# Performance work log

Hardware: AMD Instinct MI355X
Metric: run time of the kernel (lower is better)

## Reference

```python
import jax, jax.numpy as jnp
import numpy as np
from functools import partial

VOCAB = 32000
N_LAYER = 2
D_MODEL = 1024
D_INNER = 2048   # expand * d_model
D_STATE = 16
D_CONV = 4
DT_RANK = 64     # ceil(d_model/16)
SEQ_LEN = 2048   # == D_INNER (required by the repo's conv quirk)
BATCH = 1
EPS = 1e-6


def rmsnorm(x, scale):
    return x * jax.lax.rsqrt(jnp.mean(x * x, axis=-1, keepdims=True) + EPS) * scale


def setup_inputs() -> dict:
    key = jax.random.key(0)
    ks = jax.random.split(key, 16)
    s = 0.02
    L = N_LAYER
    inp = {
        "input_ids": jax.random.randint(ks[0], (BATCH, SEQ_LEN), 0, VOCAB, dtype=jnp.int32),
        "embed": jax.random.normal(ks[1], (VOCAB, D_MODEL), jnp.float32) * s,
        "norm_scale": jnp.ones((L, D_MODEL), jnp.float32),
        "in_proj_w": jax.random.normal(ks[2], (L, D_MODEL, 2 * D_INNER), jnp.float32) * s,
        "in_proj_b": jnp.zeros((L, 2 * D_INNER), jnp.float32),
        "conv_w": jax.random.normal(ks[3], (L, D_CONV, 1, SEQ_LEN), jnp.float32) * s,
        "conv_b": jnp.zeros((L, SEQ_LEN), jnp.float32),
        "x_proj_w": jax.random.normal(ks[4], (L, D_MODEL, DT_RANK + 2 * D_STATE), jnp.float32) * s,
        "dt_proj_w": jax.random.normal(ks[5], (L, DT_RANK, D_INNER), jnp.float32) * s,
        "dt_proj_b": jnp.zeros((L, D_INNER), jnp.float32),
        "out_proj_w": jax.random.normal(ks[6], (L, D_INNER, D_MODEL), jnp.float32) * s,
        "out_proj_b": jnp.zeros((L, D_MODEL), jnp.float32),
        "A_log": jnp.tile(jnp.log(jnp.arange(1, D_STATE + 1, dtype=jnp.float32)), (L, D_INNER, 1)),
        "D_param": jnp.ones((L, D_INNER), jnp.float32),
        "norm_f_scale": jnp.ones((D_MODEL,), jnp.float32),
        "lm_head_w": jax.random.normal(ks[7], (D_MODEL, VOCAB), jnp.float32) * s,
    }
    return inp


def selective_scan(u, delta, A, B, C, D):
    # u, delta: (b,l,d)   A: (d,n)   B,C: (b,l,n)   D: (d,)
    deltaA = jnp.exp(jnp.einsum('bld,dn->bldn', delta, A))            # (b,l,d,n)
    deltaB_u = delta[..., None] * B[:, :, None, :] * u[..., None]      # (b,l,d,n)

    def step(x, inps):
        dA, dBu, c = inps            # (b,d,n),(b,d,n),(b,n)
        x = dA * x + dBu
        y = jnp.einsum('bdn,bn->bd', x, c)
        return x, y

    x0 = jnp.zeros((u.shape[0], u.shape[2], A.shape[1]), u.dtype)
    _, ys = jax.lax.scan(step, x0, (jnp.moveaxis(deltaA, 1, 0),
                                    jnp.moveaxis(deltaB_u, 1, 0),
                                    jnp.moveaxis(C, 1, 0)))
    return jnp.moveaxis(ys, 0, 1) + u * D                              # (b,l,d)


def depthwise_conv(x, w, b):
    # Faithful to repo: Conv(features=SEQ_LEN, groups=D_INNER) on (b, d_inner, l).
    # With SEQ_LEN == D_INNER this is a depthwise conv over the d_inner axis.
    # x: (b, d_inner, l) as (N, W, C);  w: (d_conv, 1, SEQ_LEN)
    y = jax.lax.conv_general_dilated(x, w, window_strides=(1,), padding='SAME',
                                     dimension_numbers=('NWC', 'WIO', 'NWC'),
                                     feature_group_count=SEQ_LEN)
    return y + b


def mamba_block(h, norm_scale, in_w, in_b, conv_w, conv_b, x_proj_w,
                dt_w, dt_b, out_w, out_b, A_log, Dp):
    u = rmsnorm(h, norm_scale)
    A = -jnp.exp(A_log)
    x_and_res = u @ in_w + in_b
    x, res = jnp.split(x_and_res, 2, axis=-1)
    xt = jnp.transpose(x, (0, 2, 1))                 # (b, d_inner, l)
    xt = depthwise_conv(xt, conv_w, conv_b)[:, :, :u.shape[1]]
    x = jax.nn.silu(jnp.transpose(xt, (0, 2, 1)))     # (b, l, d_inner)
    x_dbl = u @ x_proj_w
    delta, B, C = jnp.split(x_dbl, [DT_RANK, DT_RANK + D_STATE], axis=-1)
    delta = jax.nn.softplus(delta @ dt_w + dt_b)
    y = selective_scan(x, delta, A, B, C, Dp)
    y = y * jax.nn.silu(res)
    return y @ out_w + out_b + h


def reference(input_ids, embed, norm_scale, in_proj_w, in_proj_b, conv_w, conv_b,
              x_proj_w, dt_proj_w, dt_proj_b, out_proj_w, out_proj_b, A_log,
              D_param, norm_f_scale, lm_head_w):
    h = embed[input_ids]                              # (b,l,d_model)
    for i in range(N_LAYER):
        h = mamba_block(h, norm_scale[i], in_proj_w[i], in_proj_b[i], conv_w[i],
                        conv_b[i], x_proj_w[i], dt_proj_w[i], dt_proj_b[i],
                        out_proj_w[i], out_proj_b[i], A_log[i], D_param[i])
    h = rmsnorm(h, norm_f_scale)
    return h @ lm_head_w                              # (b,l,vocab)
```

## Files before the change

kernel.cpp:

```cpp
#include <hip/hip_runtime.h>
#include <hip/hip_bf16.h>

#define SEQ 2048
#define DM  1024
#define DI  2048
#define DST 16
#define DTR 64
#define NVOC 32000
#define NVOCP 32768
#define NIN  6272
#define NC  64
#define LC  32

typedef __bf16 bf16x8 __attribute__((ext_vector_type(8)));
typedef float  f32x4  __attribute__((ext_vector_type(4)));

__device__ __forceinline__ float siluf(float x) { return x / (1.f + expf(-x)); }
__device__ __forceinline__ float softplusf(float x) {
    return fmaxf(x, 0.f) + log1pf(expf(-fabsf(x)));
}
__device__ __forceinline__ unsigned short f2bf(float f) {
    union { __hip_bfloat16 h; unsigned short u; } c;
    c.h = __float2bfloat16(f);
    return c.u;
}

__global__ void embed_gather(const int* __restrict__ ids, const float* __restrict__ embed,
                             float* __restrict__ h) {
    int l = blockIdx.x;
    int row = ids[l];
    const float4* src = (const float4*)(embed + (size_t)row * DM);
    float4* dst = (float4*)(h + (size_t)l * DM);
    dst[threadIdx.x] = src[threadIdx.x];
}

__global__ void rmsnorm_kernel(const float* __restrict__ x, const float* __restrict__ w,
                               float* __restrict__ o, unsigned short* __restrict__ ob) {
    int l = blockIdx.x;
    int t = threadIdx.x;
    float4 v = ((const float4*)(x + (size_t)l * DM))[t];
    float ss = v.x*v.x + v.y*v.y + v.z*v.z + v.w*v.w;
    #pragma unroll
    for (int m = 32; m; m >>= 1) ss += __shfl_xor(ss, m);
    __shared__ float red[4];
    if ((t & 63) == 0) red[t >> 6] = ss;
    __syncthreads();
    float tot = red[0] + red[1] + red[2] + red[3];
    float sc = rsqrtf(tot * (1.f / DM) + 1e-6f);
    float4 wv = ((const float4*)w)[t];
    float4 ov;
    ov.x = v.x * sc * wv.x;
    ov.y = v.y * sc * wv.y;
    ov.z = v.z * sc * wv.z;
    ov.w = v.w * sc * wv.w;
    if (ob) {
        uint2 pk;
        pk.x = (unsigned)f2bf(ov.x) | ((unsigned)f2bf(ov.y) << 16);
        pk.y = (unsigned)f2bf(ov.z) | ((unsigned)f2bf(ov.w) << 16);
        ((uint2*)(ob + (size_t)l * DM))[t] = pk;
    } else {
        ((float4*)(o + (size_t)l * DM))[t] = ov;
    }
}

__global__ void transpose_all(const float* __restrict__ in_w, const float* __restrict__ xp_w,
                              const float* __restrict__ out_w,
                              const float* __restrict__ lm_w,
                              unsigned short* __restrict__ in_wT, unsigned short* __restrict__ out_wT,
                              unsigned short* __restrict__ lm_wT) {
    int b = blockIdx.x;
    const float* W; unsigned short* WT; int K, N, Np, loc;
    if      (b < 1024)  { W = in_w;                        WT = in_wT;                                             K=1024; N=4096;  Np=4096;  loc = b; }
    else if (b < 1056)  { W = xp_w;                        WT = in_wT + (size_t)4096 * 1024;                       K=1024; N=96;    Np=128;   loc = b - 1024; }
    else if (b < 2080)  { W = in_w + (size_t)1024 * 4096;  WT = in_wT + (size_t)NIN * 1024;                        K=1024; N=4096;  Np=4096;  loc = b - 1056; }
    else if (b < 2112)  { W = xp_w + (size_t)1024 * 96;    WT = in_wT + (size_t)NIN * 1024 + (size_t)4096 * 1024;  K=1024; N=96;    Np=128;   loc = b - 2080; }
    else if (b < 2624)  { W = out_w;                       WT = out_wT;                                            K=2048; N=1024;  Np=1024;  loc = b - 2112; }
    else if (b < 3136)  { W = out_w + (size_t)2048 * 1024; WT = out_wT + (size_t)1024 * 2048;                      K=2048; N=1024;  Np=1024;  loc = b - 2624; }
    else                { if (!lm_wT) return; W = lm_w;    WT = lm_wT;                                             K=1024; N=32000; Np=32768; loc = b - 3136; }
    int tiles_x = Np >> 6;
    int n0 = (loc % tiles_x) * 64, k0 = (loc / tiles_x) * 64;
    __shared__ float tile[64][65];
    int t = threadIdx.y * 32 + threadIdx.x;
    {
        int kk = t >> 4;
        int n4 = (t & 15) * 4;
        #pragma unroll
        for (int i = 0; i < 4; i++) {
            int k = kk + i * 16;
            int n = n0 + n4;
            float4 v;
            if (n < N) v = *(const float4*)&W[(size_t)(k0 + k) * N + n];
            else       v = make_float4(0.f, 0.f, 0.f, 0.f);
            tile[n4 + 0][k] = v.x;
            tile[n4 + 1][k] = v.y;
            tile[n4 + 2][k] = v.z;
            tile[n4 + 3][k] = v.w;
        }
    }
    __syncthreads();
    {
        int nr = t >> 3;
        int u  = t & 7;
        #pragma unroll
        for (int pass = 0; pass < 2; pass++) {
            int nn = pass * 32 + nr;
            unsigned short tmp[8];
            #pragma unroll
            for (int j = 0; j < 8; j++) tmp[j] = f2bf(tile[nn][u * 8 + j]);
            uint4 pk;
            pk.x = (unsigned)tmp[0] | ((unsigned)tmp[1] << 16);
            pk.y = (unsigned)tmp[2] | ((unsigned)tmp[3] << 16);
            pk.z = (unsigned)tmp[4] | ((unsigned)tmp[5] << 16);
            pk.w = (unsigned)tmp[6] | ((unsigned)tmp[7] << 16);
            *(uint4*)&WT[(size_t)(n0 + nn) * K + k0 + u * 8] = pk;
        }
    }
}

__global__ __launch_bounds__(256) void compose_dtw(const float* __restrict__ xp_w,
                                                   const float* __restrict__ dt_w,
                                                   unsigned short* __restrict__ in_wT) {
    int n0 = blockIdx.x * 64, k0 = blockIdx.y * 64, L = blockIdx.z;
    const float* xp = xp_w + (size_t)L * DM * 96;
    const float* dw = dt_w + (size_t)L * DTR * DI;
    unsigned short* WT = in_wT + (size_t)L * NIN * 1024 + (size_t)4224 * 1024;
    __shared__ float xps[64][65];
    __shared__ float dts[64][65];
    int t = threadIdx.x;
    for (int i = t; i < 64 * 64; i += 256) {
        int row = i >> 6, col = i & 63;
        xps[row][col] = xp[(size_t)(k0 + row) * 96 + col];
        dts[row][col] = dw[(size_t)row * DI + n0 + col];
    }
    __syncthreads();
    int n = t & 63, kg = t >> 6;
    float acc[16] = {};
    for (int r = 0; r < 64; r++) {
        float d = dts[r][n];
        #pragma unroll
        for (int k = 0; k < 16; k++)
            acc[k] += xps[kg * 16 + k][r] * d;
    }
    #pragma unroll
    for (int k = 0; k < 16; k++)
        WT[(size_t)(n0 + n) * 1024 + k0 + kg * 16 + k] = f2bf(acc[k]);
}

template<int ACT>
__global__ __launch_bounds__(256) void gemm_f32(const float* __restrict__ A, int lda,
                                                const float* __restrict__ B,
                                                const float* __restrict__ bias,
                                                const float* __restrict__ add,
                                                float* __restrict__ C,
                                                int M, int N, int K) {
    __shared__ float As[16][68];
    __shared__ float Bs[16][64];
    int tx = threadIdx.x, ty = threadIdx.y;
    int t = ty * 16 + tx;
    int m0 = blockIdx.y * 64, n0 = blockIdx.x * 64;
    float acc[4][4] = {};
    for (int k0 = 0; k0 < K; k0 += 16) {
        #pragma unroll
        for (int i = 0; i < 4; i++) {
            int idx = t + i * 256;
            int mm = idx >> 4, kk = idx & 15;
            As[kk][mm] = A[(size_t)(m0 + mm) * lda + k0 + kk];
            int nn = idx & 63, k2 = idx >> 6;
            Bs[k2][nn] = B[(size_t)(k0 + k2) * N + n0 + nn];
        }
        __syncthreads();
        #pragma unroll
        for (int kk = 0; kk < 16; kk++) {
            float4 a = *(const float4*)&As[kk][ty * 4];
            float4 b = *(const float4*)&Bs[kk][tx * 4];
            acc[0][0] += a.x*b.x; acc[0][1] += a.x*b.y; acc[0][2] += a.x*b.z; acc[0][3] += a.x*b.w;
            acc[1][0] += a.y*b.x; acc[1][1] += a.y*b.y; acc[1][2] += a.y*b.z; acc[1][3] += a.y*b.w;
            acc[2][0] += a.z*b.x; acc[2][1] += a.z*b.y; acc[2][2] += a.z*b.z; acc[2][3] += a.z*b.w;
            acc[3][0] += a.w*b.x; acc[3][1] += a.w*b.y; acc[3][2] += a.w*b.z; acc[3][3] += a.w*b.w;
        }
        __syncthreads();
    }
    #pragma unroll
    for (int i = 0; i < 4; i++) {
        int row = m0 + ty * 4 + i;
        float4 r;
        float* pr = &r.x;
        #pragma unroll
        for (int j = 0; j < 4; j++) {
            int col = n0 + tx * 4 + j;
            float v = acc[i][j];
            if (bias) v += bias[col];
            if (add)  v += add[(size_t)row * N + col];
            if (ACT == 1) v = softplusf(v);
            pr[j] = v;
        }
        *(float4*)&C[(size_t)row * N + n0 + tx * 4] = r;
    }
}

template<int BIAS, int ADD, int ACT, int XP>
__global__ __launch_bounds__(256) void gemm_bf16(const unsigned short* __restrict__ A, int lda,
                                                 const unsigned short* __restrict__ BT,
                                                 const float* __restrict__ bias,
                                                 const float* __restrict__ add,
                                                 float* __restrict__ C,
                                                 float* __restrict__ xp_out,
                                                 float* __restrict__ dout,
                                                 const float* __restrict__ dt_bias,
                                                 int M, int N, int K) {
    __shared__ unsigned short As[128 * 32];
    __shared__ unsigned short Bs[128 * 32];
    int t = threadIdx.x;
    int w = t >> 6, l = t & 63;
    int wm = w >> 1, wn = w & 1;
    int m0 = blockIdx.x * 128;
    int n0 = blockIdx.y * 128;
    int lr = l & 15, lk = (l >> 4) * 8;
    int sr = t >> 2, sc = (t & 3) * 8;
    f32x4 acc[4][4] = {};
    for (int k0 = 0; k0 < K; k0 += 32) {
        const unsigned short* ga = A  + (size_t)(m0 + sr) * lda + k0 + sc;
        const unsigned short* gb = BT + (size_t)(n0 + sr) * K + k0 + sc;
        unsigned short* la = As + w * 512;
        unsigned short* lb = Bs + w * 512;
        __builtin_amdgcn_global_load_lds((const __attribute__((address_space(1))) void*)ga,
            (__attribute__((address_space(3))) void*)la, 16, 0, 0);
        __builtin_amdgcn_global_load_lds((const __attribute__((address_space(1))) void*)(ga + (size_t)64 * lda),
            (__attribute__((address_space(3))) void*)(la + 2048), 16, 0, 0);
        __builtin_amdgcn_global_load_lds((const __attribute__((address_space(1))) void*)gb,
            (__attribute__((address_space(3))) void*)(lb), 16, 0, 0);
        __builtin_amdgcn_global_load_lds((const __attribute__((address_space(1))) void*)(gb + (size_t)64 * K),
            (__attribute__((address_space(3))) void*)(lb + 2048), 16, 0, 0);
        __syncthreads();
        bf16x8 af[4], bfr[4];
        #pragma unroll
        for (int i = 0; i < 4; i++) {
            af[i]  = *reinterpret_cast<const bf16x8*>(&As[(wm * 64 + i * 16 + lr) * 32 + lk]);
            bfr[i] = *reinterpret_cast<const bf16x8*>(&Bs[(wn * 64 + i * 16 + lr) * 32 + lk]);
        }
        #pragma unroll
        for (int i = 0; i < 4; i++)
            #pragma unroll
            for (int j = 0; j < 4; j++)
                acc[i][j] = __builtin_amdgcn_mfma_f32_16x16x32_bf16(af[i], bfr[j], acc[i][j], 0, 0, 0);
        __syncthreads();
    }
    int cr = (l >> 4) * 4;
    if (XP && n0 >= 4224) {
        #pragma unroll
        for (int i = 0; i < 4; i++) {
            #pragma unroll
            for (int j = 0; j < 4; j++) {
                int c2 = (n0 - 4224) + wn * 64 + j * 16 + lr;
                float bv = dt_bias[c2];
                #pragma unroll
                for (int rr = 0; rr < 4; rr++) {
                    int row = m0 + wm * 64 + i * 16 + cr + rr;
                    dout[(size_t)row * DI + c2] = softplusf(acc[i][j][rr] + bv);
                }
            }
        }
    } else if (XP && n0 >= 4096) {
        #pragma unroll
        for (int i = 0; i < 4; i++) {
            #pragma unroll
            for (int j = 0; j < 4; j++) {
                int c2 = (n0 - 4096) + wn * 64 + j * 16 + lr;
                #pragma unroll
                for (int rr = 0; rr < 4; rr++) {
                    int row = m0 + wm * 64 + i * 16 + cr + rr;
                    xp_out[(size_t)row * 128 + c2] = acc[i][j][rr];
                }
            }
        }
    } else {
        int ldc = XP ? 4096 : N;
        #pragma unroll
        for (int i = 0; i < 4; i++) {
            #pragma unroll
            for (int j = 0; j < 4; j++) {
                int col = n0 + wn * 64 + j * 16 + lr;
                float bv = BIAS ? bias[col] : 0.f;
                #pragma unroll
                for (int rr = 0; rr < 4; rr++) {
                    int row = m0 + wm * 64 + i * 16 + cr + rr;
                    float v = acc[i][j][rr] + bv;
                    if (ADD) v += add[(size_t)row * ldc + col];
                    if (ACT == 1) v = softplusf(v);
                    C[(size_t)row * ldc + col] = v;
                }
            }
        }
    }
}

__global__ __launch_bounds__(1024, 4) void gemm_lm(
        const unsigned short* __restrict__ A,
        const unsigned short* __restrict__ BT,
        float* __restrict__ C, int M, int N, int K) {
    extern __shared__ unsigned short lds[];
    const int t = threadIdx.x;
    const int w = t >> 6, l = t & 63;
    const int wr = w >> 2, wc = w & 3;
    int bxx = blockIdx.x, byy = blockIdx.y;
    if (gridDim.x == 8 && (gridDim.y & 7) == 0) {
        int lin = blockIdx.y * 8 + blockIdx.x;
        int xcd = lin & 7, i = lin >> 3;
        bxx = i & 7;
        byy = xcd * (gridDim.y >> 3) + (i >> 3);
    }
    const int m0 = bxx * 256, n0 = byy * 256;
    const int lr = l & 15;
    const int rowA = wr * 64 + lr;
    const int rowB = wc * 64 + lr;
    const int colR = (((l >> 4) ^ (lr & 3)) * 8);
    const int srow = t >> 2;
    const int scol = (((t & 3) ^ (srow & 3)) * 8);
    const int NT = K >> 5;
    f32x4 acc[4][4] = {};
    bf16x8 af[4], bf[4];

    const unsigned short* gA = A  + (size_t)(m0 + srow) * K + scol;
    const unsigned short* gB = BT + (size_t)(n0 + srow) * K + scol;

    #pragma unroll
    for (int pp = 0; pp < 2; pp++) {
        if (pp < NT) {
            unsigned short* Ld = lds + pp * 16384;
            __builtin_amdgcn_global_load_lds(
                (const __attribute__((address_space(1))) void*)(gA + pp * 32),
                (__attribute__((address_space(3))) void*)(Ld + w * 512), 16, 0, 0);
            __builtin_amdgcn_global_load_lds(
                (const __attribute__((address_space(1))) void*)(gB + pp * 32),
                (__attribute__((address_space(3))) void*)(Ld + 8192 + w * 512), 16, 0, 0);
        }
    }

    for (int kt = 0; kt < NT; kt++) {
        if (kt >= NT - 2) { asm volatile("s_waitcnt vmcnt(0)" ::: "memory"); }
        else              { asm volatile("s_waitcnt vmcnt(2)" ::: "memory"); }
        __builtin_amdgcn_sched_barrier(0);
        __builtin_amdgcn_s_barrier();
        __builtin_amdgcn_sched_barrier(0);
        const unsigned short* Ab = lds + (kt % 3) * 16384;
        const unsigned short* Bb = Ab + 8192;
        #pragma unroll
        for (int i = 0; i < 4; i++)
            af[i] = *reinterpret_cast<const bf16x8*>(&Ab[(rowA + i * 16) * 32 + colR]);
        #pragma unroll
        for (int j = 0; j < 4; j++)
            bf[j] = *reinterpret_cast<const bf16x8*>(&Bb[(rowB + j * 16) * 32 + colR]);
        if (kt + 2 < NT) {
            unsigned short* Ld = lds + ((kt + 2) % 3) * 16384;
            __builtin_amdgcn_global_load_lds(
                (const __attribute__((address_space(1))) void*)(gA + (kt + 2) * 32),
                (__attribute__((address_space(3))) void*)(Ld + w * 512), 16, 0, 0);
            __builtin_amdgcn_global_load_lds(
                (const __attribute__((address_space(1))) void*)(gB + (kt + 2) * 32),
                (__attribute__((address_space(3))) void*)(Ld + 8192 + w * 512), 16, 0, 0);
        }
        __builtin_amdgcn_s_setprio(1);
        #pragma unroll
        for (int i = 0; i < 4; i++)
            #pragma unroll
            for (int j = 0; j < 4; j++)
                acc[i][j] = __builtin_amdgcn_mfma_f32_16x16x32_bf16(af[i], bf[j], acc[i][j], 0, 0, 0);
        __builtin_amdgcn_s_setprio(0);
    }

    float* cf = (float*)lds;
    const int cr = (l >> 4) * 4;
    for (int r = 0; r < 4; r++) {
        __syncthreads();
        if (wr == r) {
            #pragma unroll
            for (int i = 0; i < 4; i++)
                #pragma unroll
                for (int j = 0; j < 4; j++) {
                    int col = wc * 64 + j * 16 + lr;
                    #pragma unroll
                    for (int rr = 0; rr < 4; rr++)
                        cf[(i * 16 + cr + rr) * 260 + col] = acc[i][j][rr];
                }
        }
        __syncthreads();
        #pragma unroll
        for (int pass = 0; pass < 4; pass++) {
            int row = pass * 16 + (t >> 6);
            int f4 = t & 63;
            f32x4 v = *(const f32x4*)&cf[row * 260 + f4 * 4];
            int grow = m0 + r * 64 + row;
            int gcol = n0 + f4 * 4;
            if (gcol < N)
                __builtin_nontemporal_store(v, (f32x4*)&C[(size_t)grow * N + gcol]);
        }
    }
}

__global__ void xproj_kernel(const float* __restrict__ u, const float* __restrict__ xw,
                             float* __restrict__ xdbl) {
    int l0 = blockIdx.x * 4;
    int t = threadIdx.x;
    __shared__ float us[4][DM];
    for (int i = t; i < 4 * DM; i += 128) us[i >> 10][i & 1023] = u[(size_t)l0 * DM + i];
    __syncthreads();
    if (t < 96) {
        float a0 = 0.f, a1 = 0.f, a2 = 0.f, a3 = 0.f;
        for (int k = 0; k < DM; k++) {
            float wv = xw[(size_t)k * 96 + t];
            a0 += us[0][k] * wv; a1 += us[1][k] * wv;
            a2 += us[2][k] * wv; a3 += us[3][k] * wv;
        }
        xdbl[(size_t)(l0 + 0) * 128 + t] = a0;
        xdbl[(size_t)(l0 + 1) * 128 + t] = a1;
        xdbl[(size_t)(l0 + 2) * 128 + t] = a2;
        xdbl[(size_t)(l0 + 3) * 128 + t] = a3;
    }
}

__global__ __launch_bounds__(256) void scan_p1(const float* __restrict__ xr,
        const float* __restrict__ delta, const float* __restrict__ xdbl,
        const float* __restrict__ cw, const float* __restrict__ cb,
        const float* __restrict__ A_log, float* __restrict__ P, float* __restrict__ S) {
    int c = blockIdx.x;
    int d = blockIdx.y * 256 + threadIdx.x;
    int l0 = c * LC;
    __shared__ float Bsh[LC][16];
    __shared__ float cwsh[4][LC];
    __shared__ float cbsh[LC];
    {
        int t = threadIdx.x;
        #pragma unroll
        for (int i = t; i < LC * 16; i += 256) {
            int ll = i >> 4, q = i & 15;
            Bsh[ll][q] = xdbl[(size_t)(l0 + ll) * 128 + 64 + q];
        }
        if (t < LC) {
            cbsh[t] = cb[l0 + t];
            #pragma unroll
            for (int k = 0; k < 4; k++) cwsh[k][t] = cw[k * SEQ + l0 + t];
        }
    }
    __syncthreads();
    float a[16];
    #pragma unroll
    for (int i = 0; i < 4; i++) {
        float4 al = ((const float4*)(A_log + (size_t)d * 16))[i];
        a[4*i+0] = -expf(al.x); a[4*i+1] = -expf(al.y);
        a[4*i+2] = -expf(al.z); a[4*i+3] = -expf(al.w);
    }
    float s[16] = {};
    float sumdv = 0.f;
    for (int ll = 0; ll < LC; ll++) {
        size_t lrow = (size_t)(l0 + ll);
        float dv = delta[lrow * DI + d];
        const float* xrow = xr + lrow * 4096;
        float accv = cbsh[ll];
        #pragma unroll
        for (int k = 0; k < 4; k++) {
            int cc = d + k - 1;
            if (cc >= 0 && cc < DI) accv += xrow[cc] * cwsh[k][ll];
        }
        float xv = siluf(accv);
        float du = dv * xv;
        sumdv += dv;
        #pragma unroll
        for (int n = 0; n < 16; n++)
            s[n] = expf(dv * a[n]) * s[n] + du * Bsh[ll][n];
    }
    size_t o = ((size_t)c * DI + d) * 16;
    #pragma unroll
    for (int i = 0; i < 4; i++) {
        float4 sv = make_float4(s[4*i], s[4*i+1], s[4*i+2], s[4*i+3]);
        float4 pv = make_float4(expf(a[4*i]*sumdv), expf(a[4*i+1]*sumdv),
                                expf(a[4*i+2]*sumdv), expf(a[4*i+3]*sumdv));
        ((float4*)(S + o))[i] = sv;
        ((float4*)(P + o))[i] = pv;
    }
}

__global__ void scan_p2(const float* __restrict__ P, const float* __restrict__ S,
                        float* __restrict__ X) {
    int t = blockIdx.x * 256 + threadIdx.x;
    float x = 0.f;
    #pragma unroll 16
    for (int c = 0; c < NC; c++) {
        X[(size_t)c * (DI*16) + t] = x;
        x = P[(size_t)c * (DI*16) + t] * x + S[(size_t)c * (DI*16) + t];
    }
}

__global__ __launch_bounds__(256) void scan_p3(const float* __restrict__ xr,
        const float* __restrict__ delta, const float* __restrict__ xdbl,
        const float* __restrict__ cw, const float* __restrict__ cb,
        const float* __restrict__ A_log, const float* __restrict__ Dp,
        const float* __restrict__ X,
        float* __restrict__ y, unsigned short* __restrict__ yb) {
    int c = blockIdx.x;
    int d = blockIdx.y * 256 + threadIdx.x;
    int l0 = c * LC;
    __shared__ float Bsh[LC][16], Csh[LC][16];
    __shared__ float cwsh[4][LC];
    __shared__ float cbsh[LC];
    {
        int t = threadIdx.x;
        #pragma unroll
        for (int i = t; i < LC * 16; i += 256) {
            int ll = i >> 4, q = i & 15;
            size_t row = (size_t)(l0 + ll) * 128;
            Bsh[ll][q] = xdbl[row + 64 + q];
            Csh[ll][q] = xdbl[row + 80 + q];
        }
        if (t < LC) {
            cbsh[t] = cb[l0 + t];
            #pragma unroll
            for (int k = 0; k < 4; k++) cwsh[k][t] = cw[k * SEQ + l0 + t];
        }
    }
    __syncthreads();
    float a[16];
    #pragma unroll
    for (int i = 0; i < 4; i++) {
        float4 al = ((const float4*)(A_log + (size_t)d * 16))[i];
        a[4*i+0] = -expf(al.x); a[4*i+1] = -expf(al.y);
        a[4*i+2] = -expf(al.z); a[4*i+3] = -expf(al.w);
    }
    float s[16];
    size_t o = ((size_t)c * DI + d) * 16;
    #pragma unroll
    for (int i = 0; i < 4; i++) {
        float4 xv4 = ((const float4*)(X + o))[i];
        s[4*i] = xv4.x; s[4*i+1] = xv4.y; s[4*i+2] = xv4.z; s[4*i+3] = xv4.w;
    }
    float Dv = Dp[d];
    for (int ll = 0; ll < LC; ll++) {
        size_t lrow = (size_t)(l0 + ll);
        float dv = delta[lrow * DI + d];
        const float* xrow = xr + lrow * 4096;
        float accv = cbsh[ll];
        #pragma unroll
        for (int k = 0; k < 4; k++) {
            int cc = d + k - 1;
            if (cc >= 0 && cc < DI) accv += xrow[cc] * cwsh[k][ll];
        }
        float xv = siluf(accv);
        float du = dv * xv;
        float yv = 0.f;
        #pragma unroll
        for (int n = 0; n < 16; n++) {
            s[n] = expf(dv * a[n]) * s[n] + du * Bsh[ll][n];
            yv += s[n] * Csh[ll][n];
        }
        float res = xrow[2048 + d];
        float val = (yv + xv * Dv) * siluf(res);
        if (yb) yb[lrow * DI + d] = f2bf(val);
        else    y[lrow * DI + d] = val;
    }
}

extern "C" void kernel_launch(void* const* d_in, const int* in_sizes, int n_in,
                              void* d_out, int out_size, void* d_ws, size_t ws_size,
                              hipStream_t stream) {
    const int*   ids        = (const int*)d_in[0];
    const float* embed      = (const float*)d_in[1];
    const float* norm_scale = (const float*)d_in[2];
    const float* in_w       = (const float*)d_in[3];
    const float* in_b       = (const float*)d_in[4];
    const float* conv_w     = (const float*)d_in[5];
    const float* conv_b     = (const float*)d_in[6];
    const float* x_proj_w   = (const float*)d_in[7];
    const float* dt_w       = (const float*)d_in[8];
    const float* dt_b       = (const float*)d_in[9];
    const float* out_w      = (const float*)d_in[10];
    const float* out_b      = (const float*)d_in[11];
    const float* A_log      = (const float*)d_in[12];
    const float* Dp         = (const float*)d_in[13];
    const float* norm_f     = (const float*)d_in[14];
    const float* lm_w       = (const float*)d_in[15];

    float* out = (float*)d_out;

    char* p = (char*)d_ws;
    float* h  = (float*)p;  p += (size_t)SEQ * DM * 4;
    float* hn = (float*)p;  p += (size_t)SEQ * DM * 4;
    size_t base = (size_t)p - (size_t)d_ws;
    const size_t SZ_UB    = (size_t)SEQ * DM * 2;
    const size_t SZ_YB    = (size_t)SEQ * DI * 2;
    const size_t SZ_HNB   = (size_t)SEQ * DM * 2;
    const size_t SZ_INWT  = (size_t)2 * NIN * DM * 2;
    const size_t SZ_OUTWT = (size_t)2 * DM * DI * 2;
    const size_t SZ_LMWT  = (size_t)NVOCP * DM * 2;
    size_t need_mid  = base + SZ_UB + SZ_YB + SZ_HNB + SZ_INWT + SZ_OUTWT;
    size_t need_full = need_mid + SZ_LMWT;
    bool mid  = ws_size >= need_mid;
    bool full = ws_size >= need_full;

    unsigned short *u_b = nullptr, *y_b = nullptr, *hn_b = nullptr;
    unsigned short *in_wT = nullptr, *out_wT = nullptr, *lm_wT = nullptr;
    if (mid) {
        u_b    = (unsigned short*)p; p += SZ_UB;
        y_b    = (unsigned short*)p; p += SZ_YB;
        hn_b   = (unsigned short*)p; p += SZ_HNB;
        in_wT  = (unsigned short*)p; p += SZ_INWT;
        out_wT = (unsigned short*)p; p += SZ_OUTWT;
        if (full) { lm_wT = (unsigned short*)p; p += SZ_LMWT; }
    }

    float* u     = out;
    float* xr    = u + (size_t)SEQ * DM;
    float* xdbl  = xr + (size_t)SEQ * 4096;
    float* delta = xdbl + (size_t)SEQ * 128;
    float* y     = delta + (size_t)SEQ * DI;
    float* Pbuf  = y + (size_t)SEQ * DI;
    float* Sbuf  = Pbuf + (size_t)NC * DI * 16;
    float* Xbuf  = Sbuf + (size_t)NC * DI * 16;

    if (mid) {
        int nblocks = full ? 11328 : 3136;
        transpose_all<<<nblocks, dim3(32, 8), 0, stream>>>(
            in_w, x_proj_w, out_w, lm_w, in_wT, out_wT, lm_wT);
        compose_dtw<<<dim3(DI / 64, DM / 64, 2), 256, 0, stream>>>(
            x_proj_w, dt_w, in_wT);
    }

    embed_gather<<<SEQ, 256, 0, stream>>>(ids, embed, h);

    for (int L = 0; L < 2; L++) {
        rmsnorm_kernel<<<SEQ, 256, 0, stream>>>(h, norm_scale + (size_t)L * DM, u, u_b);
        if (mid) {
            gemm_bf16<1, 0, 0, 1><<<dim3(SEQ / 128, NIN / 128), 256, 0, stream>>>(
                u_b, DM, in_wT + (size_t)L * NIN * DM, in_b + (size_t)L * 4096, nullptr, xr,
                xdbl, delta, dt_b + (size_t)L * DI, SEQ, NIN, DM);
        } else {
            gemm_f32<0><<<dim3(4096 / 64, SEQ / 64), dim3(16, 16), 0, stream>>>(
                u, DM, in_w + (size_t)L * DM * 4096, in_b + (size_t)L * 4096, nullptr, xr,
                SEQ, 4096, DM);
            xproj_kernel<<<SEQ / 4, 128, 0, stream>>>(u, x_proj_w + (size_t)L * DM * 96, xdbl);
            gemm_f32<1><<<dim3(DI / 64, SEQ / 64), dim3(16, 16), 0, stream>>>(
                xdbl, 128, dt_w + (size_t)L * DTR * DI, dt_b + (size_t)L * DI, nullptr, delta,
                SEQ, DI, DTR);
        }
        scan_p1<<<dim3(NC, DI / 256), 256, 0, stream>>>(
            xr, delta, xdbl, conv_w + (size_t)L * 4 * SEQ, conv_b + (size_t)L * SEQ,
            A_log + (size_t)L * DI * DST, Pbuf, Sbuf);
        scan_p2<<<DI * 16 / 256, 256, 0, stream>>>(Pbuf, Sbuf, Xbuf);
        scan_p3<<<dim3(NC, DI / 256), 256, 0, stream>>>(
            xr, delta, xdbl, conv_w + (size_t)L * 4 * SEQ, conv_b + (size_t)L * SEQ,
            A_log + (size_t)L * DI * DST, Dp + (size_t)L * DI, Xbuf, y, y_b);
        if (mid) {
            gemm_bf16<1, 1, 0, 0><<<dim3(SEQ / 128, DM / 128), 256, 0, stream>>>(
                y_b, DI, out_wT + (size_t)L * DM * DI, out_b + (size_t)L * DM, h, h,
                nullptr, nullptr, nullptr, SEQ, DM, DI);
        } else {
            gemm_f32<0><<<dim3(DM / 64, SEQ / 64), dim3(16, 16), 0, stream>>>(
                y, DI, out_w + (size_t)L * DI * DM, out_b + (size_t)L * DM, h, h,
                SEQ, DM, DI);
        }
    }

    rmsnorm_kernel<<<SEQ, 256, 0, stream>>>(h, norm_f, hn, full ? hn_b : nullptr);
    if (full) {
        (void)hipFuncSetAttribute((const void*)gemm_lm,
                                  hipFuncAttributeMaxDynamicSharedMemorySize, 98304);
        gemm_lm<<<dim3(SEQ / 256, NVOCP / 256), 1024, 98304, stream>>>(
            hn_b, lm_wT, out, SEQ, NVOC, DM);
    } else {
        gemm_f32<0><<<dim3(NVOC / 64, SEQ / 64), dim3(16, 16), 0, stream>>>(
            hn, DM, lm_w, nullptr, nullptr, out, SEQ, NVOC, DM);
    }
}
```

Baseline: 744.7 us.

## Route fused in_proj/x_proj/dt GEMM through the 256-tile LM-head kernel

The fused input projection GEMM (in_proj, x_proj and composed dt_proj columns) now uses the 256x256-tile, 1024-thread kernel previously used only for the LM head. That kernel is templated with an epilogue that adds bias, splits columns into xr, xdbl and softplus delta. The packed weight width is padded from 6272 to 6400 columns to fit 256-wide tiles, and the old 128-tile kernel loses its split-output epilogue. The aim is better data reuse and MFMA throughput on a large GEMM, at the cost of a grid of only 200 large blocks and some wasted padded columns.

```diff
diff --git a/kernel.cpp b/kernel.cpp
--- a/kernel.cpp
+++ b/kernel.cpp
@@ -9,6 +9,7 @@
 #define NVOC 32000
 #define NVOCP 32768
 #define NIN  6272
+#define NINP 6400
 #define NC  64
 #define LC  32
 
@@ -70,13 +71,13 @@
                               unsigned short* __restrict__ lm_wT) {
     int b = blockIdx.x;
     const float* W; unsigned short* WT; int K, N, Np, loc;
-    if      (b < 1024)  { W = in_w;                        WT = in_wT;                                             K=1024; N=4096;  Np=4096;  loc = b; }
-    else if (b < 1056)  { W = xp_w;                        WT = in_wT + (size_t)4096 * 1024;                       K=1024; N=96;    Np=128;   loc = b - 1024; }
-    else if (b < 2080)  { W = in_w + (size_t)1024 * 4096;  WT = in_wT + (size_t)NIN * 1024;                        K=1024; N=4096;  Np=4096;  loc = b - 1056; }
-    else if (b < 2112)  { W = xp_w + (size_t)1024 * 96;    WT = in_wT + (size_t)NIN * 1024 + (size_t)4096 * 1024;  K=1024; N=96;    Np=128;   loc = b - 2080; }
-    else if (b < 2624)  { W = out_w;                       WT = out_wT;                                            K=2048; N=1024;  Np=1024;  loc = b - 2112; }
-    else if (b < 3136)  { W = out_w + (size_t)2048 * 1024; WT = out_wT + (size_t)1024 * 2048;                      K=2048; N=1024;  Np=1024;  loc = b - 2624; }
-    else                { if (!lm_wT) return; W = lm_w;    WT = lm_wT;                                             K=1024; N=32000; Np=32768; loc = b - 3136; }
+    if      (b < 1024)  { W = in_w;                        WT = in_wT;                                              K=1024; N=4096;  Np=4096;  loc = b; }
+    else if (b < 1056)  { W = xp_w;                        WT = in_wT + (size_t)4096 * 1024;                        K=1024; N=96;    Np=128;   loc = b - 1024; }
+    else if (b < 2080)  { W = in_w + (size_t)1024 * 4096;  WT = in_wT + (size_t)NINP * 1024;                        K=1024; N=4096;  Np=4096;  loc = b - 1056; }
+    else if (b < 2112)  { W = xp_w + (size_t)1024 * 96;    WT = in_wT + (size_t)NINP * 1024 + (size_t)4096 * 1024;  K=1024; N=96;    Np=128;   loc = b - 2080; }
+    else if (b < 2624)  { W = out_w;                       WT = out_wT;                                             K=2048; N=1024;  Np=1024;  loc = b - 2112; }
+    else if (b < 3136)  { W = out_w + (size_t)2048 * 1024; WT = out_wT + (size_t)1024 * 2048;                       K=2048; N=1024;  Np=1024;  loc = b - 2624; }
+    else                { if (!lm_wT) return; W = lm_w;    WT = lm_wT;                                              K=1024; N=32000; Np=32768; loc = b - 3136; }
     int tiles_x = Np >> 6;
     int n0 = (loc % tiles_x) * 64, k0 = (loc / tiles_x) * 64;
     __shared__ float tile[64][65];
@@ -123,7 +124,7 @@
     int n0 = blockIdx.x * 64, k0 = blockIdx.y * 64, L = blockIdx.z;
     const float* xp = xp_w + (size_t)L * DM * 96;
     const float* dw = dt_w + (size_t)L * DTR * DI;
-    unsigned short* WT = in_wT + (size_t)L * NIN * 1024 + (size_t)4224 * 1024;
+    unsigned short* WT = in_wT + (size_t)L * NINP * 1024 + (size_t)4224 * 1024;
     __shared__ float xps[64][65];
     __shared__ float dts[64][65];
     int t = threadIdx.x;
@@ -198,15 +199,12 @@
     }
 }
 
-template<int BIAS, int ADD, int ACT, int XP>
+template<int BIAS, int ADD, int ACT>
 __global__ __launch_bounds__(256) void gemm_bf16(const unsigned short* __restrict__ A, int lda,
                                                  const unsigned short* __restrict__ BT,
                                                  const float* __restrict__ bias,
                                                  const float* __restrict__ add,
                                                  float* __restrict__ C,
-                                                 float* __restrict__ xp_out,
-                                                 float* __restrict__ dout,
-                                                 const float* __restrict__ dt_bias,
                                                  int M, int N, int K) {
     __shared__ unsigned short As[128 * 32];
     __shared__ unsigned short Bs[128 * 32];
@@ -246,58 +244,32 @@
         __syncthreads();
     }
     int cr = (l >> 4) * 4;
-    if (XP && n0 >= 4224) {
-        #pragma unroll
-        for (int i = 0; i < 4; i++) {
+    #pragma unroll
+    for (int i = 0; i < 4; i++) {
+        #pragma unroll
+        for (int j = 0; j < 4; j++) {
+            int col = n0 + wn * 64 + j * 16 + lr;
+            float bv = BIAS ? bias[col] : 0.f;
             #pragma unroll
-            for (int j = 0; j < 4; j++) {
-                int c2 = (n0 - 4224) + wn * 64 + j * 16 + lr;
-                float bv = dt_bias[c2];
-                #pragma unroll
-                for (int rr = 0; rr < 4; rr++) {
-                    int row = m0 + wm * 64 + i * 16 + cr + rr;
-                    dout[(size_t)row * DI + c2] = softplusf(acc[i][j][rr] + bv);
-                }
+            for (int rr = 0; rr < 4; rr++) {
+                int row = m0 + wm * 64 + i * 16 + cr + rr;
+                float v = acc[i][j][rr] + bv;
+                if (ADD) v += add[(size_t)row * N + col];
+                if (ACT == 1) v = softplusf(v);
+                C[(size_t)row * N + col] = v;
             }
         }
-    } else if (XP && n0 >= 4096) {
-        #pragma unroll
-        for (int i = 0; i < 4; i++) {
-            #pragma unroll
-            for (int j = 0; j < 4; j++) {
-                int c2 = (n0 - 4096) + wn * 64 + j * 16 + lr;
-                #pragma unroll
-                for (int rr = 0; rr < 4; rr++) {
-                    int row = m0 + wm * 64 + i * 16 + cr + rr;
-                    xp_out[(size_t)row * 128 + c2] = acc[i][j][rr];
-                }
-            }
-        }
-    } else {
-        int ldc = XP ? 4096 : N;
-        #pragma unroll
-        for (int i = 0; i < 4; i++) {
-            #pragma unroll
-            for (int j = 0; j < 4; j++) {
-                int col = n0 + wn * 64 + j * 16 + lr;
-                float bv = BIAS ? bias[col] : 0.f;
-                #pragma unroll
-                for (int rr = 0; rr < 4; rr++) {
-                    int row = m0 + wm * 64 + i * 16 + cr + rr;
-                    float v = acc[i][j][rr] + bv;
-                    if (ADD) v += add[(size_t)row * ldc + col];
-                    if (ACT == 1) v = softplusf(v);
-                    C[(size_t)row * ldc + col] = v;
-                }
-            }
-        }
-    }
-}
-
-__global__ __launch_bounds__(1024, 4) void gemm_lm(
+    }
+}
+
+template<int EPI>
+__global__ __launch_bounds__(1024, 4) void gemm_256(
         const unsigned short* __restrict__ A,
         const unsigned short* __restrict__ BT,
-        float* __restrict__ C, int M, int N, int K) {
+        float* __restrict__ C, const float* __restrict__ bias,
+        float* __restrict__ xp_out, float* __restrict__ dout,
+        const float* __restrict__ dt_bias,
+        int M, int N, int K) {
     extern __shared__ unsigned short lds[];
     const int t = threadIdx.x;
     const int w = t >> 6, l = t & 63;
@@ -391,8 +363,27 @@
             f32x4 v = *(const f32x4*)&cf[row * 260 + f4 * 4];
             int grow = m0 + r * 64 + row;
             int gcol = n0 + f4 * 4;
-            if (gcol < N)
-                __builtin_nontemporal_store(v, (f32x4*)&C[(size_t)grow * N + gcol]);
+            if (EPI == 0) {
+                if (gcol < N)
+                    __builtin_nontemporal_store(v, (f32x4*)&C[(size_t)grow * N + gcol]);
+            } else {
+                if (gcol < 4096) {
+                    const f32x4 bv = *(const f32x4*)&bias[gcol];
+                    v += bv;
+                    *(f32x4*)&C[(size_t)grow * 4096 + gcol] = v;
+                } else if (gcol < 4224) {
+                    *(f32x4*)&xp_out[(size_t)grow * 128 + (gcol - 4096)] = v;
+                } else if (gcol < NIN) {
+                    int c2 = gcol - 4224;
+                    const f32x4 bv = *(const f32x4*)&dt_bias[c2];
+                    f32x4 o;
+                    o[0] = softplusf(v[0] + bv[0]);
+                    o[1] = softplusf(v[1] + bv[1]);
+                    o[2] = softplusf(v[2] + bv[2]);
+                    o[3] = softplusf(v[3] + bv[3]);
+                    *(f32x4*)&dout[(size_t)grow * DI + c2] = o;
+                }
+            }
         }
     }
 }
@@ -587,7 +578,7 @@
     const size_t SZ_UB    = (size_t)SEQ * DM * 2;
     const size_t SZ_YB    = (size_t)SEQ * DI * 2;
     const size_t SZ_HNB   = (size_t)SEQ * DM * 2;
-    const size_t SZ_INWT  = (size_t)2 * NIN * DM * 2;
+    const size_t SZ_INWT  = (size_t)2 * NINP * DM * 2;
     const size_t SZ_OUTWT = (size_t)2 * DM * DI * 2;
     const size_t SZ_LMWT  = (size_t)NVOCP * DM * 2;
     size_t need_mid  = base + SZ_UB + SZ_YB + SZ_HNB + SZ_INWT + SZ_OUTWT;
@@ -621,6 +612,10 @@
             in_w, x_proj_w, out_w, lm_w, in_wT, out_wT, lm_wT);
         compose_dtw<<<dim3(DI / 64, DM / 64, 2), 256, 0, stream>>>(
             x_proj_w, dt_w, in_wT);
+        (void)hipFuncSetAttribute((const void*)gemm_256<0>,
+                                  hipFuncAttributeMaxDynamicSharedMemorySize, 98304);
+        (void)hipFuncSetAttribute((const void*)gemm_256<1>,
+                                  hipFuncAttributeMaxDynamicSharedMemorySize, 98304);
     }
 
     embed_gather<<<SEQ, 256, 0, stream>>>(ids, embed, h);
@@ -628,9 +623,9 @@
     for (int L = 0; L < 2; L++) {
         rmsnorm_kernel<<<SEQ, 256, 0, stream>>>(h, norm_scale + (size_t)L * DM, u, u_b);
         if (mid) {
-            gemm_bf16<1, 0, 0, 1><<<dim3(SEQ / 128, NIN / 128), 256, 0, stream>>>(
-                u_b, DM, in_wT + (size_t)L * NIN * DM, in_b + (size_t)L * 4096, nullptr, xr,
-                xdbl, delta, dt_b + (size_t)L * DI, SEQ, NIN, DM);
+            gemm_256<1><<<dim3(SEQ / 256, NINP / 256), 1024, 98304, stream>>>(
+                u_b, in_wT + (size_t)L * NINP * DM, xr, in_b + (size_t)L * 4096,
+                xdbl, delta, dt_b + (size_t)L * DI, SEQ, NINP, DM);
         } else {
             gemm_f32<0><<<dim3(4096 / 64, SEQ / 64), dim3(16, 16), 0, stream>>>(
                 u, DM, in_w + (size_t)L * DM * 4096, in_b + (size_t)L * 4096, nullptr, xr,
@@ -648,9 +643,9 @@
             xr, delta, xdbl, conv_w + (size_t)L * 4 * SEQ, conv_b + (size_t)L * SEQ,
             A_log + (size_t)L * DI * DST, Dp + (size_t)L * DI, Xbuf, y, y_b);
         if (mid) {
-            gemm_bf16<1, 1, 0, 0><<<dim3(SEQ / 128, DM / 128), 256, 0, stream>>>(
+            gemm_bf16<1, 1, 0><<<dim3(SEQ / 128, DM / 128), 256, 0, stream>>>(
                 y_b, DI, out_wT + (size_t)L * DM * DI, out_b + (size_t)L * DM, h, h,
-                nullptr, nullptr, nullptr, SEQ, DM, DI);
+                SEQ, DM, DI);
         } else {
             gemm_f32<0><<<dim3(DM / 64, SEQ / 64), dim3(16, 16), 0, stream>>>(
                 y, DI, out_w + (size_t)L * DI * DM, out_b + (size_t)L * DM, h, h,
@@ -660,10 +655,8 @@
 
     rmsnorm_kernel<<<SEQ, 256, 0, stream>>>(h, norm_f, hn, full ? hn_b : nullptr);
     if (full) {
-        (void)hipFuncSetAttribute((const void*)gemm_lm,
-                                  hipFuncAttributeMaxDynamicSharedMemorySize, 98304);
-        gemm_lm<<<dim3(SEQ / 256, NVOCP / 256), 1024, 98304, stream>>>(
-            hn_b, lm_wT, out, SEQ, NVOC, DM);
+        gemm_256<0><<<dim3(SEQ / 256, NVOCP / 256), 1024, 98304, stream>>>(
+            hn_b, lm_wT, out, nullptr, nullptr, nullptr, nullptr, SEQ, NVOC, DM);
     } else {
         gemm_f32<0><<<dim3(NVOC / 64, SEQ / 64), dim3(16, 16), 0, stream>>>(
             hn, DM, lm_w, nullptr, nullptr, out, SEQ, NVOC, DM);
```

New measurement: 736.2 us. Within noise of the previous version (-1.1%).
